# Optimization experiments

Measured on AMD Instinct MI355X. Metric: run time of the kernel, lower is better.

The kernel has to match this reference:

```python
import jax, jax.numpy as jnp
import numpy as np

DECAY = 0.2
THRESH = 0.8


def setup_inputs() -> dict:
    key = jax.random.key(0)
    ks = jax.random.split(key, 5)
    B, T, Cin, H, W = 16, 15, 64, 56, 56
    Cout = 128
    x = jax.random.normal(ks[0], (B, T, Cin, H, W), dtype=jnp.float32)
    # torch conv init then *5; random normal scaled similarly
    fan_in = Cin * 3 * 3
    conv_w = jax.random.normal(ks[1], (Cout, Cin, 3, 3), dtype=jnp.float32) * (5.0 / np.sqrt(fan_in))
    conv_b = jax.random.normal(ks[2], (Cout,), dtype=jnp.float32) * (1.0 / np.sqrt(fan_in))
    fc_w = jax.random.normal(ks[3], (1, 3), dtype=jnp.float32) * (1.0 / np.sqrt(3.0))
    fc_b = jax.random.normal(ks[4], (1,), dtype=jnp.float32) * (1.0 / np.sqrt(3.0))
    return {"x": x, "conv_w": conv_w, "conv_b": conv_b, "fc_w": fc_w, "fc_b": fc_b, "wins": 15}


def _act_fun(v):
    # step function (surrogate gradient only matters in bwd module)
    return (v > 0.0).astype(v.dtype)


def _conv(x_t, conv_w, conv_b):
    out = jax.lax.conv_general_dilated(
        x_t, conv_w, window_strides=(1, 1), padding=((1, 1), (1, 1)),
        dimension_numbers=("NCHW", "OIHW", "NCHW"))
    return out + conv_b[None, :, None, None]


def _fc(m3, fc_w, fc_b):
    # Linear(3,1) over last axis: [B,C,H,W,3] -> [B,C,H,W]
    return jnp.einsum("bchwi,i->bchw", m3, fc_w[0]) + fc_b[0]


def _avg_pool2(s):
    B, C, H, W = s.shape
    return s.reshape(B, C, H // 2, 2, W // 2, 2).mean(axis=(3, 5))


def reference(x, conv_w, conv_b, fc_w, fc_b, wins):
    B, T, Cin, H, W = x.shape
    Cout = conv_w.shape[0]
    mem0 = jnp.zeros((B, Cout, H, W, 4), dtype=x.dtype)
    spike0 = jnp.zeros((B, Cout, H, W), dtype=x.dtype)

    def step(carry, x_t):
        mem, spike = carry
        conv_out = _conv(x_t, conv_w, conv_b)  # [B,Cout,H,W]
        # inner input computed from OLD mem channels 0:3 (matches update_neuron)
        x4 = _fc(mem[..., 0:3], fc_w, fc_b)
        decayed = mem * (DECAY * (1.0 - spike))[..., None]
        new03 = decayed[..., 0:3] + conv_out[..., None]
        new3 = decayed[..., 3] + x4
        mem_new = jnp.concatenate([new03, new3[..., None]], axis=-1)
        mem1 = _fc(mem_new[..., 0:3], fc_w, fc_b) + mem_new[..., 3]
        spike_new = _act_fun(mem1 - THRESH)
        return (mem_new, spike_new), _avg_pool2(spike_new)

    xs = jnp.transpose(x[:, :wins], (1, 0, 2, 3, 4))  # [T,B,Cin,H,W]
    _, spikes = jax.lax.scan(step, (mem0, spike0), xs)
    return jnp.transpose(spikes, (1, 0, 2, 3, 4))  # [B,T,Cout,H/2,W/2]
```

## Files before the change

kernel.cpp:

```cpp
#include <hip/hip_runtime.h>

#define B_N 16
#define T_N 15
#define CIN 64
#define COUT 128
#define HS 56
#define HWN 3136
#define NSG (16 * 128 * 28 * 28)


__global__ void wt_kernel(const float* __restrict__ w, float* __restrict__ wt4) {
    int i = blockIdx.x * 256 + threadIdx.x;
    if (i >= COUT * 576) return;
    int co = i / 576;
    int r = i - co * 576;
    int ci = r / 9;
    int kk = r - ci * 9;
    wt4[((size_t)kk * CIN + ci) * COUT + co] = w[i];
}

__global__ __launch_bounds__(256) void conv_sgpr(
    const float* __restrict__ x, const float* __restrict__ wt4,
    const float* __restrict__ bias, float* __restrict__ obuf,
    int t0, int nz)
{
    __shared__ float xs[CIN * 100];

    const int bid = blockIdx.x;
    const int z = (bid & 7) * (nz >> 3) + (bid >> 3);

    const int tile = z % 49;
    const int u = z / 49;
    const int b = u & 15;
    const int tc = u >> 4;

    const int ty = tile / 7, tx = tile - ty * 7;
    const int h0 = ty * 8, w0c = tx * 8;

    const int tid = threadIdx.x;

    const float* xb = x + ((size_t)(b * T_N + (t0 + tc)) * CIN) * HWN;
    for (int i = tid; i < CIN * 100; i += 256) {
        int ci = i / 100;
        int rem = i - ci * 100;
        int rr = rem / 10;
        int cc = rem - rr * 10;
        int gh = h0 - 1 + rr;
        int gw = w0c - 1 + cc;
        float v = 0.0f;
        if ((unsigned)gh < (unsigned)HS && (unsigned)gw < (unsigned)HS)
            v = xb[(size_t)ci * HWN + gh * HS + gw];
        xs[i] = v;
    }
    __syncthreads();

    const int lane = tid & 63;
    const int wv = __builtin_amdgcn_readfirstlane(tid >> 6);
    const int co0 = wv * 32;
    const int lh = lane >> 3;
    const int lw = lane & 7;

    float acc[32];
#pragma unroll
    for (int j = 0; j < 32; ++j) acc[j] = 0.0f;

    for (int kh = 0; kh < 3; ++kh) {
        for (int kw = 0; kw < 3; ++kw) {
            const int xoff = (lh + kh) * 10 + (lw + kw);
            const float* wk = wt4 + ((size_t)(kh * 3 + kw) * CIN) * COUT + co0;
            for (int c8 = 0; c8 < 8; ++c8) {
                float xv[8];
#pragma unroll
                for (int k = 0; k < 8; ++k)
                    xv[k] = xs[(c8 * 8 + k) * 100 + xoff];
#pragma unroll
                for (int k = 0; k < 8; ++k) {
                    const int ci = c8 * 8 + k;
#pragma unroll
                    for (int j = 0; j < 32; ++j) {
                        acc[j] = fmaf(xv[k], wk[ci * COUT + j], acc[j]);
                    }
                }
            }
        }
    }

    const int h = h0 + lh;
    const int wq = w0c + lw;
    const size_t obase = ((size_t)(tc * 16 + b) * COUT + co0) * HWN
                       + (size_t)h * HS + wq;
#pragma unroll
    for (int j = 0; j < 32; ++j) {
        obuf[obase + (size_t)j * HWN] = __fadd_rn(acc[j], bias[co0 + j]);
    }
}

__global__ __launch_bounds__(256) void rec32(
    const float* __restrict__ cvbuf, const float* __restrict__ fcw,
    const float* __restrict__ fcb, float* __restrict__ stateD,
    unsigned* __restrict__ stateS, float* __restrict__ out,
    int t0, int nt, int doLoad, int doStore)
{
    const int idx = blockIdx.x * 256 + threadIdx.x;
    const int pw = idx % 28;
    int tmp = idx / 28;
    const int ph = tmp % 28;
    tmp /= 28;
    const int co = tmp & 127;
    const int b = tmp >> 7;

    const size_t g = (size_t)idx;

    const float w0 = fcw[0], w1 = fcw[1], w2 = fcw[2], fb = fcb[0];

    float u[4], m3[4], s[4];
    if (doLoad) {
        unsigned sm = stateS[g];
#pragma unroll
        for (int p = 0; p < 4; ++p) {
            u[p] = stateD[(size_t)p * NSG + g];
            m3[p] = stateD[(size_t)(4 + p) * NSG + g];
            s[p] = (float)((sm >> p) & 1u);
        }
    } else {
#pragma unroll
        for (int p = 0; p < 4; ++p) { u[p] = 0.0f; m3[p] = 0.0f; s[p] = 0.0f; }
    }

    const int h0 = ph * 2, wc0 = pw * 2;

    for (int tc = 0; tc < nt; ++tc) {
        const size_t cbase = ((size_t)(tc * 16 + b) * COUT + co) * HWN
                           + (size_t)h0 * HS + wc0;
        const float cv[4] = {cvbuf[cbase], cvbuf[cbase + 1],
                             cvbuf[cbase + HS], cvbuf[cbase + HS + 1]};

#pragma unroll
        for (int p = 0; p < 4; ++p) {
            float e0 = __fadd_rn(__fadd_rn(__fmul_rn(u[p], w0), __fmul_rn(u[p], w1)),
                                 __fmul_rn(u[p], w2));
            float x4 = __fadd_rn(e0, fb);
            float dd = __fmul_rn(0.2f, __fsub_rn(1.0f, s[p]));
            u[p]  = __fadd_rn(__fmul_rn(u[p], dd), cv[p]);
            m3[p] = __fadd_rn(__fmul_rn(m3[p], dd), x4);
            float e1 = __fadd_rn(__fadd_rn(__fmul_rn(u[p], w0), __fmul_rn(u[p], w1)),
                                 __fmul_rn(u[p], w2));
            float mem1 = __fadd_rn(__fadd_rn(e1, fb), m3[p]);
            s[p] = (__fsub_rn(mem1, 0.8f) > 0.0f) ? 1.0f : 0.0f;
        }

        float pooled = 0.25f * (((s[0] + s[1]) + s[2]) + s[3]);
        out[(((size_t)b * T_N + (t0 + tc)) * COUT + co) * 784 + ph * 28 + pw] = pooled;
    }

    if (doStore) {
        unsigned sm = 0;
#pragma unroll
        for (int p = 0; p < 4; ++p) {
            stateD[(size_t)p * NSG + g] = u[p];
            stateD[(size_t)(4 + p) * NSG + g] = m3[p];
            sm |= (s[p] > 0.5f) ? (1u << p) : 0u;
        }
        stateS[g] = sm;
    }
}

extern "C" void kernel_launch(void* const* d_in, const int* in_sizes, int n_in,
                              void* d_out, int out_size, void* d_ws, size_t ws_size,
                              hipStream_t stream) {
    const float* x     = (const float*)d_in[0];
    const float* cw    = (const float*)d_in[1];
    const float* cbias = (const float*)d_in[2];
    const float* fcw   = (const float*)d_in[3];
    const float* fcb   = (const float*)d_in[4];
    float* out = (float*)d_out;

    const size_t wtB   = (size_t)576 * COUT * sizeof(float);
    const size_t convT = (size_t)B_N * COUT * HWN * sizeof(float);
    const size_t statB = (size_t)NSG * 8 * sizeof(float)
                       + (size_t)NSG * sizeof(unsigned);

    int Tc;
    if (wtB + (size_t)T_N * convT <= ws_size) {
        Tc = T_N;
    } else if (ws_size > wtB + statB + convT) {
        Tc = (int)((ws_size - wtB - statB) / convT);
        if (Tc > T_N) Tc = T_N;
    } else {
        return;
    }

    float* wt4 = (float*)d_ws;
    float* convbuf = (float*)((char*)d_ws + wtB);
    float* stateD = (float*)((char*)d_ws + wtB + (size_t)Tc * convT);
    unsigned* stateS = (unsigned*)((char*)stateD + (size_t)NSG * 8 * sizeof(float));

    wt_kernel<<<(COUT * 576 + 255) / 256, 256, 0, stream>>>(cw, wt4);

    for (int t0 = 0; t0 < T_N; t0 += Tc) {
        const int nt = (T_N - t0 < Tc) ? (T_N - t0) : Tc;
        const int nz = nt * 16 * 49;
        conv_sgpr<<<nz, 256, 0, stream>>>(x, wt4, cbias, convbuf, t0, nz);
        rec32<<<NSG / 256, 256, 0, stream>>>(
            convbuf, fcw, fcb, stateD, stateS, out,
            t0, nt, t0 > 0 ? 1 : 0, (t0 + nt) < T_N ? 1 : 0);
    }
}
```

Baseline: 1.441 ms.

## Stage conv weights in LDS and use 4x4 register tiles per thread

Rewrites the conv kernel so each block computes half of the output channels. Per tap, weights are staged into LDS in channel-minor order, and the input tile is stored with ci innermost and padded to 68. Each thread computes a 4-channel by 4-pixel register tile using float4 LDS reads, instead of 32 channels for one pixel with weights streamed from global/scalar loads. The grid doubles, so input tile loads are duplicated across the two channel halves, and there are extra syncthreads per tap.

```diff
diff --git a/kernel.cpp b/kernel.cpp
--- a/kernel.cpp
+++ b/kernel.cpp
@@ -7,6 +7,7 @@
 #define HS 56
 #define HWN 3136
 #define NSG (16 * 128 * 28 * 28)
+#define XP 68
 
 
 __global__ void wt_kernel(const float* __restrict__ w, float* __restrict__ wt4) {
@@ -19,79 +20,109 @@
     wt4[((size_t)kk * CIN + ci) * COUT + co] = w[i];
 }
 
-__global__ __launch_bounds__(256) void conv_sgpr(
+__global__ __launch_bounds__(256) void conv_lds2(
     const float* __restrict__ x, const float* __restrict__ wt4,
     const float* __restrict__ bias, float* __restrict__ obuf,
     int t0, int nz)
 {
-    __shared__ float xs[CIN * 100];
+    __shared__ float xs[100 * XP];
+    __shared__ float wl[64 * XP];
 
     const int bid = blockIdx.x;
     const int z = (bid & 7) * (nz >> 3) + (bid >> 3);
 
-    const int tile = z % 49;
-    const int u = z / 49;
+    const int coh = z & 1;
+    int u = z >> 1;
+    const int tile = u % 49;
+    u /= 49;
     const int b = u & 15;
     const int tc = u >> 4;
 
-    const int ty = tile / 7, tx = tile - ty * 7;
-    const int h0 = ty * 8, w0c = tx * 8;
-
+    const int h0 = (tile / 7) * 8, w0c = (tile % 7) * 8;
     const int tid = threadIdx.x;
 
     const float* xb = x + ((size_t)(b * T_N + (t0 + tc)) * CIN) * HWN;
     for (int i = tid; i < CIN * 100; i += 256) {
         int ci = i / 100;
         int rem = i - ci * 100;
-        int rr = rem / 10;
-        int cc = rem - rr * 10;
-        int gh = h0 - 1 + rr;
-        int gw = w0c - 1 + cc;
+        int rr = rem / 10, cc = rem - rr * 10;
+        int gh = h0 - 1 + rr, gw = w0c - 1 + cc;
         float v = 0.0f;
         if ((unsigned)gh < (unsigned)HS && (unsigned)gw < (unsigned)HS)
             v = xb[(size_t)ci * HWN + gh * HS + gw];
-        xs[i] = v;
-    }
-    __syncthreads();
-
-    const int lane = tid & 63;
-    const int wv = __builtin_amdgcn_readfirstlane(tid >> 6);
-    const int co0 = wv * 32;
-    const int lh = lane >> 3;
-    const int lw = lane & 7;
-
-    float acc[32];
-#pragma unroll
-    for (int j = 0; j < 32; ++j) acc[j] = 0.0f;
-
-    for (int kh = 0; kh < 3; ++kh) {
-        for (int kw = 0; kw < 3; ++kw) {
-            const int xoff = (lh + kh) * 10 + (lw + kw);
-            const float* wk = wt4 + ((size_t)(kh * 3 + kw) * CIN) * COUT + co0;
-            for (int c8 = 0; c8 < 8; ++c8) {
-                float xv[8];
-#pragma unroll
-                for (int k = 0; k < 8; ++k)
-                    xv[k] = xs[(c8 * 8 + k) * 100 + xoff];
-#pragma unroll
-                for (int k = 0; k < 8; ++k) {
-                    const int ci = c8 * 8 + k;
-#pragma unroll
-                    for (int j = 0; j < 32; ++j) {
-                        acc[j] = fmaf(xv[k], wk[ci * COUT + j], acc[j]);
+        xs[rem * XP + ci] = v;
+    }
+
+    const int cog = tid >> 4;
+    const int pxg = tid & 15;
+    const int co0l = cog * 4;
+    const int px0 = pxg * 4;
+    const int lh = px0 >> 3;
+    const int lw0 = px0 & 7;
+
+    const int ciw = tid >> 4;
+    const int cl4 = tid & 15;
+
+    float acc[4][4];
+#pragma unroll
+    for (int j = 0; j < 4; ++j)
+#pragma unroll
+        for (int p = 0; p < 4; ++p) acc[j][p] = 0.0f;
+
+    for (int tap = 0; tap < 9; ++tap) {
+        __syncthreads();
+#pragma unroll
+        for (int k2 = 0; k2 < 4; ++k2) {
+            const int ci = ciw * 4 + k2;
+            const float4 wv = *(const float4*)(
+                wt4 + ((size_t)tap * CIN + ci) * COUT + coh * 64 + cl4 * 4);
+            wl[(cl4 * 4 + 0) * XP + ci] = wv.x;
+            wl[(cl4 * 4 + 1) * XP + ci] = wv.y;
+            wl[(cl4 * 4 + 2) * XP + ci] = wv.z;
+            wl[(cl4 * 4 + 3) * XP + ci] = wv.w;
+        }
+        __syncthreads();
+
+        const int kh = tap / 3, kw = tap - kh * 3;
+        const int xoff = (lh + kh) * 10 + (lw0 + kw);
+
+        for (int c4 = 0; c4 < 16; ++c4) {
+            float4 xq[4], wq[4];
+#pragma unroll
+            for (int p = 0; p < 4; ++p)
+                xq[p] = *(const float4*)&xs[(xoff + p) * XP + c4 * 4];
+#pragma unroll
+            for (int j = 0; j < 4; ++j)
+                wq[j] = *(const float4*)&wl[(co0l + j) * XP + c4 * 4];
+#pragma unroll
+            for (int k = 0; k < 4; ++k) {
+#pragma unroll
+                for (int j = 0; j < 4; ++j) {
+                    const float wjk = (k == 0) ? wq[j].x : (k == 1) ? wq[j].y
+                                    : (k == 2) ? wq[j].z : wq[j].w;
+#pragma unroll
+                    for (int p = 0; p < 4; ++p) {
+                        const float xpk = (k == 0) ? xq[p].x : (k == 1) ? xq[p].y
+                                        : (k == 2) ? xq[p].z : xq[p].w;
+                        acc[j][p] = fmaf(xpk, wjk, acc[j][p]);
                     }
                 }
             }
         }
     }
 
-    const int h = h0 + lh;
-    const int wq = w0c + lw;
-    const size_t obase = ((size_t)(tc * 16 + b) * COUT + co0) * HWN
-                       + (size_t)h * HS + wq;
-#pragma unroll
-    for (int j = 0; j < 32; ++j) {
-        obuf[obase + (size_t)j * HWN] = __fadd_rn(acc[j], bias[co0 + j]);
+    const size_t btc = (size_t)(tc * 16 + b);
+#pragma unroll
+    for (int j = 0; j < 4; ++j) {
+        const int co = coh * 64 + co0l + j;
+        const float bv = bias[co];
+        float4 o;
+        o.x = __fadd_rn(acc[j][0], bv);
+        o.y = __fadd_rn(acc[j][1], bv);
+        o.z = __fadd_rn(acc[j][2], bv);
+        o.w = __fadd_rn(acc[j][3], bv);
+        *(float4*)(obuf + (btc * COUT + co) * HWN
+                   + (size_t)(h0 + lh) * HS + (w0c + lw0)) = o;
     }
 }
 
@@ -199,8 +230,8 @@
 
     for (int t0 = 0; t0 < T_N; t0 += Tc) {
         const int nt = (T_N - t0 < Tc) ? (T_N - t0) : Tc;
-        const int nz = nt * 16 * 49;
-        conv_sgpr<<<nz, 256, 0, stream>>>(x, wt4, cbias, convbuf, t0, nz);
+        const int nz = nt * 16 * 49 * 2;
+        conv_lds2<<<nz, 256, 0, stream>>>(x, wt4, cbias, convbuf, t0, nz);
         rec32<<<NSG / 256, 256, 0, stream>>>(
             convbuf, fcw, fcb, stateD, stateS, out,
             t0, nt, t0 > 0 ? 1 : 0, (t0 + nt) < T_N ? 1 : 0);
```

Measured after the change: 2.655 ms. 1.84x slower.
